# Optimization experiments

Hardware: AMD Instinct MI355X
Metric: run time of the kernel (lower is better)

Reference implementation:

```python
import jax, jax.numpy as jnp
import numpy as np

B, S, E, H = 1, 8192, 1024, 16
D = E // H
SEG_LENS = [2048, 4096, 8192]
DILATIONS = [1, 2, 4]


def setup_inputs() -> dict:
    key = jax.random.key(0)
    k0, k1, k2 = jax.random.split(key, 3)
    sc_in = 1.0 / np.sqrt(E)
    return {
        "x": jax.random.normal(k0, (B, S, E), jnp.float32),
        "w_qkv": jax.random.normal(k1, (3 * E, E), jnp.float32) * sc_in,
        "b_qkv": jnp.zeros((3 * E,), jnp.float32),
        "w_out": jax.random.normal(k2, (E, E), jnp.float32) * sc_in,
        "b_out": jnp.zeros((E,), jnp.float32),
    }


def _sdpa(q, k, v):
    # q,k,v: [B,H,N,D]; standard scaled dot-product attention (non-causal)
    scale = 1.0 / np.sqrt(q.shape[-1])
    scores = jnp.einsum('bhqd,bhkd->bhqk', q, k) * scale
    probs = jax.nn.softmax(scores, axis=-1)
    return jnp.einsum('bhqk,bhkd->bhqd', probs, v)


def reference(x, w_qkv, b_qkv, w_out, b_out):
    # QKV projection: torch Linear is x @ W^T + b
    qkv = x @ w_qkv.T + b_qkv                       # [B,S,3E]
    qkv = qkv.reshape(B, S, 3, H, D).transpose(2, 0, 3, 1, 4)  # [3,B,H,S,D]
    q, k, v = qkv[0], qkv[1], qkv[2]

    seg_outputs = []
    for seg_len, dil in zip(SEG_LENS, DILATIONS):
        if seg_len > S:
            continue
        if dil > 1:
            n = min(seg_len, S // dil)
            pos = np.arange(0, n * dil, dil)        # strided dilated gather
        else:
            pos = np.arange(seg_len)                # leading segment
        o = _sdpa(q[:, :, pos], k[:, :, pos], v[:, :, pos])
        # scatter back to full length (zero elsewhere); also handles zero-padding
        full = jnp.zeros((B, H, S, D), x.dtype).at[:, :, pos, :].set(o)
        seg_outputs.append(full)

    if len(seg_outputs) == 0:
        out = jnp.zeros((B, H, S, D), x.dtype)
    else:
        out = seg_outputs[0]
        for so in seg_outputs[1:]:
            out = out + so
        out = out / len(seg_outputs)                # stack(...).mean(0)

    out = out.transpose(0, 2, 1, 3).reshape(B, S, E)
    return out @ w_out.T + b_out
```

## Files before the change

### kernel.cpp

```cpp
#include <hip/hip_runtime.h>


typedef __attribute__((ext_vector_type(8))) short bf16x8;
typedef __attribute__((ext_vector_type(4))) float f32x4;

#define MFMA(a, b, c) __builtin_amdgcn_mfma_f32_16x16x32_bf16((a), (b), (c), 0, 0, 0)

#if __has_builtin(__builtin_amdgcn_exp2f)
#define EXP2(x) __builtin_amdgcn_exp2f(x)
#else
#define EXP2(x) exp2f(x)
#endif

static __device__ __forceinline__ unsigned short f2bf(float f) {
  unsigned int u = __float_as_uint(f);
  unsigned int r = (u + 0x7FFFu + ((u >> 16) & 1u)) >> 16;
  return (unsigned short)r;
}

__global__ void cvt_f32_bf16(const float* __restrict__ in,
                             unsigned short* __restrict__ out, int n8) {
  int i = blockIdx.x * blockDim.x + threadIdx.x;
  if (i >= n8) return;
  const float4* p = (const float4*)in + (size_t)i * 2;
  float4 a = p[0];
  float4 b = p[1];
  union { bf16x8 v; unsigned short u[8]; } o;
  o.u[0] = f2bf(a.x); o.u[1] = f2bf(a.y); o.u[2] = f2bf(a.z); o.u[3] = f2bf(a.w);
  o.u[4] = f2bf(b.x); o.u[5] = f2bf(b.y); o.u[6] = f2bf(b.z); o.u[7] = f2bf(b.w);
  *((bf16x8*)out + i) = o.v;
}

template <int EPILOGUE>
__global__ __launch_bounds__(256, 2) void gemm_bt(
    const unsigned short* __restrict__ A, const unsigned short* __restrict__ B,
    const float* __restrict__ bias, void* __restrict__ Cout, int N, int K) {
  __shared__ unsigned short At[128 * 32];
  __shared__ unsigned short Bt[128 * 32];
  const int tid = threadIdx.x;
  const int wave = tid >> 6, lane = tid & 63;
  const int quad = lane >> 4, lc = lane & 15;
  const int wm = (wave >> 1) * 64, wn = (wave & 1) * 64;
  const int m0 = blockIdx.x * 128, n0 = blockIdx.y * 128;

  f32x4 acc[4][4] = {};

  for (int k0 = 0; k0 < K; k0 += 32) {
    __syncthreads();
#pragma unroll
    for (int issue = 0; issue < 2; ++issue) {
      const int cbase = issue * 256 + wave * 64;
      const int c = cbase + lane;
      const int row = c >> 2, col8 = (c & 3) * 8;
      __builtin_amdgcn_global_load_lds(
          (const __attribute__((address_space(1))) void*)&A[(size_t)(m0 + row) * K + k0 + col8],
          (__attribute__((address_space(3))) void*)&At[cbase * 8], 16, 0, 0);
      __builtin_amdgcn_global_load_lds(
          (const __attribute__((address_space(1))) void*)&B[(size_t)(n0 + row) * K + k0 + col8],
          (__attribute__((address_space(3))) void*)&Bt[cbase * 8], 16, 0, 0);
    }
    __syncthreads();
    bf16x8 af[4], bfr[4];
#pragma unroll
    for (int t = 0; t < 4; ++t)
      af[t] = *(const bf16x8*)&At[(wm + t * 16 + lc) * 32 + quad * 8];
#pragma unroll
    for (int t = 0; t < 4; ++t)
      bfr[t] = *(const bf16x8*)&Bt[(wn + t * 16 + lc) * 32 + quad * 8];
#pragma unroll
    for (int i = 0; i < 4; ++i)
#pragma unroll
      for (int j = 0; j < 4; ++j)
        acc[i][j] = MFMA(af[i], bfr[j], acc[i][j]);
  }

#pragma unroll
  for (int i = 0; i < 4; ++i) {
#pragma unroll
    for (int j = 0; j < 4; ++j) {
      const int gcol = n0 + wn + j * 16 + lc;
      const float bs = bias[gcol];
#pragma unroll
      for (int r = 0; r < 4; ++r) {
        const int grow = m0 + wm + i * 16 + quad * 4 + r;
        const float v = acc[i][j][r] + bs;
        if (EPILOGUE == 0) {
          const int which = gcol >> 10, rem = gcol & 1023;
          const int hh = rem >> 6, d = rem & 63;
          const float vs = (which == 0) ? v * 0.18033688f : v;
          ((unsigned short*)Cout)[(((size_t)(which * 16 + hh)) * 8192 + grow) * 64 + d] = f2bf(vs);
        } else {
          ((float*)Cout)[(size_t)grow * N + gcol] = v;
        }
      }
    }
  }
}

__global__ void transpose_v(const unsigned short* __restrict__ v,
                            unsigned short* __restrict__ vt1,
                            unsigned short* __restrict__ vt2,
                            unsigned short* __restrict__ vt3) {
  __shared__ unsigned short Tt[64 * 72];
  const int tid = threadIdx.x;
  const int h = blockIdx.y;
  const int bx = blockIdx.x;
  const unsigned short* src = v + (size_t)h * 8192 * 64;
  unsigned short* dst;
  int dil, Nk, t0;
  if (bx < 32)      { dst = vt1; dil = 1; Nk = 2048; t0 = bx; }
  else if (bx < 96) { dst = vt2; dil = 2; Nk = 4096; t0 = bx - 32; }
  else              { dst = vt3; dil = 4; Nk = 2048; t0 = bx - 96; }
  dst += (size_t)h * 64 * Nk;
  const int j0 = t0 * 64;
#pragma unroll
  for (int it = 0; it < 2; ++it) {
    const int slot = tid + it * 256;
    const int jj = slot >> 3, c8 = (slot & 7) * 8;
    *(bf16x8*)&Tt[jj * 72 + c8] =
        *(const bf16x8*)&src[(size_t)(j0 + jj) * dil * 64 + c8];
  }
  __syncthreads();
  const int d = tid >> 2, pg = (tid & 3) * 16;
  union { bf16x8 v2[2]; unsigned short u[16]; } ob;
#pragma unroll
  for (int t = 0; t < 16; ++t) {
    const int pos = pg + t;
    const int w = pos & 31;
    const int jj = (pos & 32) | (((w >> 2) & 1) * 16 + (w >> 3) * 4 + (w & 3));
    ob.u[t] = Tt[jj * 72 + d];
  }
  *(bf16x8*)&dst[(size_t)d * Nk + j0 + pg] = ob.v2[0];
  *(bf16x8*)&dst[(size_t)d * Nk + j0 + pg + 8] = ob.v2[1];
}

__global__ __launch_bounds__(512, 2) void flash_all(
    const unsigned short* __restrict__ qkvb,
    const unsigned short* __restrict__ vt1, float* __restrict__ o1,
    const unsigned short* __restrict__ vt2, float* __restrict__ o2,
    const unsigned short* __restrict__ vt3, float* __restrict__ o3) {
  __shared__ unsigned short Smem[2 * 8192 + 128];

  const int bx = blockIdx.x;
  int z, h, qt;
  if ((bx & 1) == 0) { const int i = bx >> 1; z = 1; h = i >> 4; qt = i & 15; }
  else { const int j = bx >> 1; z = (j & 1) ? 2 : 0; const int i = j >> 1; h = i >> 3; qt = i & 7; }
  const int Nk = (z == 1) ? 4096 : 2048;
  const int dil = 1 << z;
  const unsigned short* vt = (z == 0) ? vt1 : (z == 1) ? vt2 : vt3;
  float* o = (z == 0) ? o1 : (z == 1) ? o2 : o3;

  const int tid = threadIdx.x;
  const int wave = tid >> 6, lane = tid & 63;
  const int quad = lane >> 4, lc = lane & 15;
  const int ks = wave >> 2, wq = wave & 3;

  const unsigned short* qh = qkvb + (size_t)h * 8192 * 64;
  const unsigned short* kh = qkvb + (size_t)(16 + h) * 8192 * 64;
  const unsigned short* vh = vt + (size_t)h * 64 * Nk;

  bf16x8 qf[4][2];
#pragma unroll
  for (int mb = 0; mb < 4; ++mb) {
    const size_t qrow = (size_t)(qt * 256 + wq * 64 + mb * 16 + lc) * dil;
    qf[mb][0] = *(const bf16x8*)&qh[qrow * 64 + quad * 8];
    qf[mb][1] = *(const bf16x8*)&qh[qrow * 64 + quad * 8 + 32];
  }

  f32x4 oacc[4][4] = {};
  float lsum[4] = {0.f, 0.f, 0.f, 0.f};

  const int srow = wave * 8 + (lane >> 3);
  const int kchunk = (lane & 7) ^ (srow & 7);

#define STAGE(kbv, b)                                                          \
  do {                                                                         \
    const int _kb = (kbv);                                                     \
    __builtin_amdgcn_global_load_lds(                                          \
        (const __attribute__((address_space(1))) void*)                        \
            &kh[(size_t)((_kb + srow) * dil) * 64 + kchunk * 8],               \
        (__attribute__((address_space(3))) void*)&Smem[(b) * 8192 + wave * 512], \
        16, 0, 0);                                                             \
    __builtin_amdgcn_global_load_lds(                                          \
        (const __attribute__((address_space(1))) void*)                        \
            &vh[(size_t)srow * Nk + _kb + kchunk * 8],                         \
        (__attribute__((address_space(3))) void*)&Smem[(b) * 8192 + 4096 + wave * 512], \
        16, 0, 0);                                                             \
  } while (0)

  STAGE(0, 0);
  __syncthreads();

  for (int kb = 0, t = 0; kb < Nk; kb += 64, ++t) {
    const int cur = t & 1;
    if (kb + 64 < Nk) STAGE(kb + 64, cur ^ 1);
    const unsigned short* Kt = &Smem[cur * 8192];
    const unsigned short* Vt = &Smem[cur * 8192 + 4096];

    union { unsigned int u[4]; bf16x8 v; } pb[4];
#pragma unroll
    for (int t2 = 0; t2 < 2; ++t2) {
      const int row = (ks * 2 + t2) * 16 + lc;
      const bf16x8 ka0 = *(const bf16x8*)&Kt[row * 64 + ((quad ^ (lc & 7)) * 8)];
      const bf16x8 ka1 = *(const bf16x8*)&Kt[row * 64 + (((4 + quad) ^ (lc & 7)) * 8)];
#pragma unroll
      for (int mb = 0; mb < 4; ++mb) {
        f32x4 zz = {};
        zz = MFMA(ka0, qf[mb][0], zz);
        zz = MFMA(ka1, qf[mb][1], zz);
        const unsigned int a0 = __float_as_uint(EXP2(zz[0])) + 0x8000u;
        const unsigned int a1 = __float_as_uint(EXP2(zz[1])) + 0x8000u;
        const unsigned int a2 = __float_as_uint(EXP2(zz[2])) + 0x8000u;
        const unsigned int a3 = __float_as_uint(EXP2(zz[3])) + 0x8000u;
        pb[mb].u[t2 * 2 + 0] = __builtin_amdgcn_perm(a1, a0, 0x07060302u);
        pb[mb].u[t2 * 2 + 1] = __builtin_amdgcn_perm(a3, a2, 0x07060302u);
        lsum[mb] += (__uint_as_float(a0 & 0xFFFF0000u) + __uint_as_float(a1 & 0xFFFF0000u)) +
                    (__uint_as_float(a2 & 0xFFFF0000u) + __uint_as_float(a3 & 0xFFFF0000u));
      }
    }

    __builtin_amdgcn_s_setprio(1);
#pragma unroll
    for (int nb = 0; nb < 4; ++nb) {
      const int vrow = nb * 16 + lc;
      const bf16x8 va = *(const bf16x8*)&Vt[vrow * 64 + (((ks * 4 + quad) ^ (lc & 7)) * 8)];
#pragma unroll
      for (int mb = 0; mb < 4; ++mb)
        oacc[mb][nb] = MFMA(va, pb[mb].v, oacc[mb][nb]);
    }
    __builtin_amdgcn_s_setprio(0);

    __syncthreads();
  }

#pragma unroll
  for (int mb = 0; mb < 4; ++mb) {
    lsum[mb] += __shfl_xor(lsum[mb], 16, 64);
    lsum[mb] += __shfl_xor(lsum[mb], 32, 64);
  }

  float* Wo = (float*)Smem + wq * 16 * 64;
  float* Wp = (float*)Smem + 4096 + wq * 16 * 64;
  float* lbuf = (float*)Smem + 8192;
  const int g = lane >> 2, s4 = lane & 3;
#pragma unroll
  for (int mb = 0; mb < 4; ++mb) {
    if (wave >= 4) {
#pragma unroll
      for (int nb = 0; nb < 4; ++nb) {
        const int c = nb * 4 + quad;
        const int cs = (c & 8) | ((c & 7) ^ (lc & 7));
        *(f32x4*)&Wp[lc * 64 + cs * 4] = oacc[mb][nb];
      }
      if (quad == 0) lbuf[wq * 16 + lc] = lsum[mb];
    }
    __syncthreads();
    if (wave < 4) {
      const float inv = 1.0f / (3.0f * (lsum[mb] + lbuf[wq * 16 + lc]));
#pragma unroll
      for (int nb = 0; nb < 4; ++nb) {
        const int c = nb * 4 + quad;
        const int cs = (c & 8) | ((c & 7) ^ (lc & 7));
        f32x4 val = oacc[mb][nb] + *(const f32x4*)&Wp[lc * 64 + cs * 4];
        val *= inv;
        *(f32x4*)&Wo[lc * 64 + cs * 4] = val;
      }
      const size_t base = (size_t)(qt * 256 + wq * 64 + mb * 16 + g) * 1024 +
                          (size_t)h * 64 + s4 * 16;
#pragma unroll
      for (int c2 = 0; c2 < 4; ++c2) {
        const int c = s4 * 4 + c2;
        const int cs = (c & 8) | ((c & 7) ^ (g & 7));
        *(float4*)&o[base + c2 * 4] = *(const float4*)&Wo[g * 64 + cs * 4];
      }
    }
    __syncthreads();
  }
#undef STAGE
}

__global__ void combine(const float* __restrict__ o1, const float* __restrict__ o2,
                        const float* __restrict__ o3,
                        unsigned short* __restrict__ a3b) {
  const int idx = blockIdx.x * 256 + threadIdx.x;
  const int s = idx >> 7, e = (idx & 127) * 8;
  float acc[8] = {};
  if (s < 2048) {
    const float* p = &o1[(size_t)s * 1024 + e];
#pragma unroll
    for (int t = 0; t < 8; ++t) acc[t] += p[t];
  }
  if (!(s & 1)) {
    const float* p = &o2[(size_t)(s >> 1) * 1024 + e];
#pragma unroll
    for (int t = 0; t < 8; ++t) acc[t] += p[t];
  }
  if (!(s & 3)) {
    const float* p = &o3[(size_t)(s >> 2) * 1024 + e];
#pragma unroll
    for (int t = 0; t < 8; ++t) acc[t] += p[t];
  }
  union { bf16x8 v; unsigned short u[8]; } ob;
#pragma unroll
  for (int t = 0; t < 8; ++t) ob.u[t] = f2bf(acc[t]);
  *(bf16x8*)&a3b[(size_t)s * 1024 + e] = ob.v;
}

extern "C" void kernel_launch(void* const* d_in, const int* in_sizes, int n_in,
                              void* d_out, int out_size, void* d_ws, size_t ws_size,
                              hipStream_t stream) {
  const float* x     = (const float*)d_in[0];
  const float* w_qkv = (const float*)d_in[1];
  const float* b_qkv = (const float*)d_in[2];
  const float* w_out = (const float*)d_in[3];
  const float* b_out = (const float*)d_in[4];
  float* out = (float*)d_out;

  char* ws = (char*)d_ws;
  unsigned short* qkvb  = (unsigned short*)(ws);
  float*          o1    = (float*)(ws + 33554432);
  float*          o3    = (float*)(ws + 41943040);
  unsigned short* vt1   = (unsigned short*)(ws + 50331648);
  unsigned short* vt2   = (unsigned short*)(ws + 54525952);
  unsigned short* vt3   = (unsigned short*)(ws + 62914560);
  float*          o2    = (float*)(ws + 67108864);
  unsigned short* wqkvb = (unsigned short*)(ws + 83886080);
  unsigned short* woutb = (unsigned short*)(ws + 90177536);
  unsigned short* xb    = (unsigned short*)(ws + 92274688);
  unsigned short* a3b   = xb;

  cvt_f32_bf16<<<dim3(8388608 / 8 / 256), dim3(256), 0, stream>>>(x, xb, 8388608 / 8);
  cvt_f32_bf16<<<dim3(3145728 / 8 / 256), dim3(256), 0, stream>>>(w_qkv, wqkvb, 3145728 / 8);
  cvt_f32_bf16<<<dim3(1048576 / 8 / 256), dim3(256), 0, stream>>>(w_out, woutb, 1048576 / 8);

  gemm_bt<0><<<dim3(64, 24), dim3(256), 0, stream>>>(xb, wqkvb, b_qkv, qkvb, 3072, 1024);

  transpose_v<<<dim3(128, 16), dim3(256), 0, stream>>>(qkvb + (size_t)32 * 8192 * 64,
                                                       vt1, vt2, vt3);

  flash_all<<<dim3(512), dim3(512), 0, stream>>>(qkvb, vt1, o1, vt2, o2, vt3, o3);

  combine<<<dim3(4096), dim3(256), 0, stream>>>(o1, o2, o3, a3b);

  gemm_bt<1><<<dim3(64, 8), dim3(256), 0, stream>>>(a3b, woutb, b_out, out, 1024, 1024);
}
```

Measured before the change: 369.4 us.

## Triple-buffer K/V staging, compute row sums via MFMA, use packed bf16 convert

Moves the K/V LDS staging from double to triple buffering with a prefetch distance of two tiles. The per-iteration __syncthreads is replaced by explicit vmcnt waits plus s_barrier, and the load addresses are advanced incrementally. Softmax denominators are now accumulated with an extra MFMA against a vector of ones instead of scalar adds and end-of-loop shuffles. The probabilities are packed with v_cvt_pk_bf16_f32 instead of manual rounding. The cost is more LDS per block, which could reduce occupancy at 2 blocks per CU, and four extra MFMAs per tile.

```diff
diff --git a/kernel.cpp b/kernel.cpp
--- a/kernel.cpp
+++ b/kernel.cpp
@@ -139,7 +139,7 @@
     const unsigned short* __restrict__ vt1, float* __restrict__ o1,
     const unsigned short* __restrict__ vt2, float* __restrict__ o2,
     const unsigned short* __restrict__ vt3, float* __restrict__ o3) {
-  __shared__ unsigned short Smem[2 * 8192 + 128];
+  __shared__ unsigned short Smem[3 * 8192 + 128];
 
   const int bx = blockIdx.x;
   int z, h, qt;
@@ -167,35 +167,46 @@
     qf[mb][1] = *(const bf16x8*)&qh[qrow * 64 + quad * 8 + 32];
   }
 
+  union { bf16x8 v; unsigned short u[8]; } one_u;
+#pragma unroll
+  for (int t = 0; t < 8; ++t) one_u.u[t] = 0x3F80;
+  const bf16x8 vone = one_u.v;
+
   f32x4 oacc[4][4] = {};
-  float lsum[4] = {0.f, 0.f, 0.f, 0.f};
+  f32x4 lacc[4] = {};
 
   const int srow = wave * 8 + (lane >> 3);
   const int kchunk = (lane & 7) ^ (srow & 7);
-
-#define STAGE(kbv, b)                                                          \
+  const size_t kstep = (size_t)64 * dil * 64;
+  const unsigned short* kp = &kh[(size_t)(srow * dil) * 64 + kchunk * 8];
+  const unsigned short* vp = &vh[(size_t)srow * Nk + kchunk * 8];
+
+#define STAGE(b)                                                               \
   do {                                                                         \
-    const int _kb = (kbv);                                                     \
     __builtin_amdgcn_global_load_lds(                                          \
-        (const __attribute__((address_space(1))) void*)                        \
-            &kh[(size_t)((_kb + srow) * dil) * 64 + kchunk * 8],               \
+        (const __attribute__((address_space(1))) void*)kp,                     \
         (__attribute__((address_space(3))) void*)&Smem[(b) * 8192 + wave * 512], \
         16, 0, 0);                                                             \
     __builtin_amdgcn_global_load_lds(                                          \
-        (const __attribute__((address_space(1))) void*)                        \
-            &vh[(size_t)srow * Nk + _kb + kchunk * 8],                         \
+        (const __attribute__((address_space(1))) void*)vp,                     \
         (__attribute__((address_space(3))) void*)&Smem[(b) * 8192 + 4096 + wave * 512], \
         16, 0, 0);                                                             \
+    kp += kstep;                                                               \
+    vp += 64;                                                                  \
   } while (0)
 
-  STAGE(0, 0);
-  __syncthreads();
-
-  for (int kb = 0, t = 0; kb < Nk; kb += 64, ++t) {
-    const int cur = t & 1;
-    if (kb + 64 < Nk) STAGE(kb + 64, cur ^ 1);
-    const unsigned short* Kt = &Smem[cur * 8192];
-    const unsigned short* Vt = &Smem[cur * 8192 + 4096];
+  const int NT = Nk >> 6;
+  STAGE(0);
+  STAGE(1);
+  asm volatile("s_waitcnt vmcnt(2)" ::: "memory");
+  __builtin_amdgcn_s_barrier();
+  __builtin_amdgcn_sched_barrier(0);
+
+  int bR = 0, bS = 2;
+  for (int t = 0; t < NT; ++t) {
+    if (t + 2 < NT) STAGE(bS);
+    const unsigned short* Kt = &Smem[bR * 8192];
+    const unsigned short* Vt = &Smem[bR * 8192 + 4096];
 
     union { unsigned int u[4]; bf16x8 v; } pb[4];
 #pragma unroll
@@ -208,14 +219,15 @@
         f32x4 zz = {};
         zz = MFMA(ka0, qf[mb][0], zz);
         zz = MFMA(ka1, qf[mb][1], zz);
-        const unsigned int a0 = __float_as_uint(EXP2(zz[0])) + 0x8000u;
-        const unsigned int a1 = __float_as_uint(EXP2(zz[1])) + 0x8000u;
-        const unsigned int a2 = __float_as_uint(EXP2(zz[2])) + 0x8000u;
-        const unsigned int a3 = __float_as_uint(EXP2(zz[3])) + 0x8000u;
-        pb[mb].u[t2 * 2 + 0] = __builtin_amdgcn_perm(a1, a0, 0x07060302u);
-        pb[mb].u[t2 * 2 + 1] = __builtin_amdgcn_perm(a3, a2, 0x07060302u);
-        lsum[mb] += (__uint_as_float(a0 & 0xFFFF0000u) + __uint_as_float(a1 & 0xFFFF0000u)) +
-                    (__uint_as_float(a2 & 0xFFFF0000u) + __uint_as_float(a3 & 0xFFFF0000u));
+        const float e0 = EXP2(zz[0]);
+        const float e1 = EXP2(zz[1]);
+        const float e2 = EXP2(zz[2]);
+        const float e3 = EXP2(zz[3]);
+        unsigned int p01, p23;
+        asm("v_cvt_pk_bf16_f32 %0, %1, %2" : "=v"(p01) : "v"(e0), "v"(e1));
+        asm("v_cvt_pk_bf16_f32 %0, %1, %2" : "=v"(p23) : "v"(e2), "v"(e3));
+        pb[mb].u[t2 * 2 + 0] = p01;
+        pb[mb].u[t2 * 2 + 1] = p23;
       }
     }
 
@@ -228,17 +240,21 @@
       for (int mb = 0; mb < 4; ++mb)
         oacc[mb][nb] = MFMA(va, pb[mb].v, oacc[mb][nb]);
     }
+#pragma unroll
+    for (int mb = 0; mb < 4; ++mb) lacc[mb] = MFMA(vone, pb[mb].v, lacc[mb]);
     __builtin_amdgcn_s_setprio(0);
 
-    __syncthreads();
-  }
-
-#pragma unroll
-  for (int mb = 0; mb < 4; ++mb) {
-    lsum[mb] += __shfl_xor(lsum[mb], 16, 64);
-    lsum[mb] += __shfl_xor(lsum[mb], 32, 64);
-  }
-
+    if (t + 1 < NT) {
+      if (t + 2 < NT) asm volatile("s_waitcnt vmcnt(2)" ::: "memory");
+      else            asm volatile("s_waitcnt vmcnt(0)" ::: "memory");
+      __builtin_amdgcn_s_barrier();
+      __builtin_amdgcn_sched_barrier(0);
+    }
+    bR = (bR == 2) ? 0 : bR + 1;
+    bS = (bS == 2) ? 0 : bS + 1;
+  }
+
+  __syncthreads();
   float* Wo = (float*)Smem + wq * 16 * 64;
   float* Wp = (float*)Smem + 4096 + wq * 16 * 64;
   float* lbuf = (float*)Smem + 8192;
@@ -252,11 +268,11 @@
         const int cs = (c & 8) | ((c & 7) ^ (lc & 7));
         *(f32x4*)&Wp[lc * 64 + cs * 4] = oacc[mb][nb];
       }
-      if (quad == 0) lbuf[wq * 16 + lc] = lsum[mb];
+      if (quad == 0) lbuf[wq * 16 + lc] = lacc[mb][0];
     }
     __syncthreads();
     if (wave < 4) {
-      const float inv = 1.0f / (3.0f * (lsum[mb] + lbuf[wq * 16 + lc]));
+      const float inv = 1.0f / (3.0f * (lacc[mb][0] + lbuf[wq * 16 + lc]));
 #pragma unroll
       for (int nb = 0; nb < 4; ++nb) {
         const int c = nb * 4 + quad;
```

After: 347.0 us. 1.06x faster.
